# Kernel optimization log

Hardware: AMD Instinct MI355X
Metric: run time of the kernel (lower is better)

The kernel has to match this reference:

```python
import jax, jax.numpy as jnp
import numpy as np

N = 50000      # nodes
E = 800000     # edges (before self-loops)
F_IN = 64      # num_features
HID = 32       # hidden_channels
HEADS = 4
CLS = 3
NEG_SLOPE = 0.2  # PyG GATConv default


def setup_inputs() -> dict:
    key = jax.random.key(0)
    ks = jax.random.split(key, 12)
    s = 0.1
    return {
        "x": jax.random.normal(ks[0], (N, F_IN), jnp.float32),
        "W1": jax.random.normal(ks[1], (F_IN, HEADS * HID), jnp.float32) * s,
        "att_src1": jax.random.normal(ks[2], (HEADS, HID), jnp.float32) * s,
        "att_dst1": jax.random.normal(ks[3], (HEADS, HID), jnp.float32) * s,
        "b1": jnp.zeros((HEADS * HID,), jnp.float32),
        "W2": jax.random.normal(ks[4], (HEADS * HID, HID), jnp.float32) * s,
        "att_src2": jax.random.normal(ks[5], (1, HID), jnp.float32) * s,
        "att_dst2": jax.random.normal(ks[6], (1, HID), jnp.float32) * s,
        "b2": jnp.zeros((HID,), jnp.float32),
        "linW": jax.random.normal(ks[7], (HID, CLS), jnp.float32) * s,
        "linb": jnp.zeros((CLS,), jnp.float32),
        "edge_index": jax.random.randint(ks[8], (2, E), 0, N, dtype=jnp.int64),
    }


def _gat_conv(x, W, att_src, att_dst, bias, src, dst, heads):
    """PyG GATConv (eval mode, self-loops pre-added in src/dst)."""
    n = x.shape[0]
    h = (x @ W).reshape(n, heads, -1)                      # [N,H,C]
    a_src = jnp.sum(h * att_src, axis=-1)                  # [N,H]
    a_dst = jnp.sum(h * att_dst, axis=-1)                  # [N,H]
    e = jax.nn.leaky_relu(a_src[src] + a_dst[dst], NEG_SLOPE)  # [E,H]
    # segment softmax over destination node
    m = jax.ops.segment_max(e, dst, num_segments=n)
    p = jnp.exp(e - m[dst])
    denom = jax.ops.segment_sum(p, dst, num_segments=n)
    alpha = p / denom[dst]                                 # [E,H]
    msg = h[src] * alpha[:, :, None]                       # [E,H,C]
    out = jax.ops.segment_sum(msg, dst, num_segments=n)    # [N,H,C]
    return out.reshape(n, -1) + bias                       # concat heads


def reference(x, W1, att_src1, att_dst1, b1, W2, att_src2, att_dst2, b2, linW, linb, edge_index):
    n = x.shape[0]
    loop = jnp.arange(n, dtype=edge_index.dtype)
    src = jnp.concatenate([edge_index[0], loop])  # add self-loops (PyG default)
    dst = jnp.concatenate([edge_index[1], loop])
    h = _gat_conv(x, W1, att_src1, att_dst1, b1, src, dst, HEADS)
    h = jax.nn.elu(h)
    h = _gat_conv(h, W2, att_src2, att_dst2, b2, src, dst, 1)
    g = jnp.mean(h, axis=0, keepdims=True)        # batch is None path
    logits = g @ linW + linb                      # [1, CLS]
    return jax.nn.softmax(logits, axis=1)
```

## Files before the change

### kernel.cpp

```cpp
#include <hip/hip_runtime.h>
#include <hip/hip_fp16.h>
#include <math.h>

#define NEG_SLOPE 0.2f
#define CAP 64
#define SCB 2048

static __device__ __forceinline__ void atomAdd(float* a, float v) {
    unsafeAtomicAdd(a, v);
}

static __device__ __forceinline__ bool edges_are_i64(const int* __restrict__ ei) {
    return (ei[1] | ei[3] | ei[5] | ei[7]) == 0;
}
static __device__ __forceinline__ int ldsrc(const int* __restrict__ ei, int e, int E, bool i64) {
    return i64 ? ei[2 * e] : ei[e];
}
static __device__ __forceinline__ int lddst(const int* __restrict__ ei, int e, int E, bool i64) {
    return i64 ? ei[2 * (E + e)] : ei[E + e];
}

__global__ __launch_bounds__(256) void scatter_k(const int* __restrict__ ei,
                                                 int* __restrict__ deg,
                                                 int* __restrict__ col, int E, int N) {
    const int tid = threadIdx.x;
    const int grp = blockIdx.x & 3;
    const int bin = blockIdx.x >> 2;
    const int nb  = gridDim.x >> 2;
    const bool i64 = edges_are_i64(ei);
    const int ET = E + N;
    const int d0 = (int)((long long)grp * N / 4);
    const int d1 = (int)((long long)(grp + 1) * N / 4);
    for (int e = bin * 256 + tid; e < ET; e += nb * 256) {
        int s, d;
        if (e < E) { s = ldsrc(ei, e, E, i64); d = lddst(ei, e, E, i64); }
        else       { s = d = e - E; }
        if (d >= d0 && d < d1) {
            int pos = atomicAdd(&deg[d], 1);
            if (pos < CAP) col[d * CAP + pos] = s;
        }
    }
}

__global__ __launch_bounds__(256, 4) void gemm1_k(const float* __restrict__ x,
                                                  const float* __restrict__ W,
                                                  const float* __restrict__ aws,
                                                  const float* __restrict__ awd,
                                                  __half* __restrict__ h,
                                                  float* __restrict__ as_,
                                                  float* __restrict__ ad_, int N) {
    __shared__ float Ws[64 * 128];
    __shared__ float xs[32 * 64];
    const int tid = threadIdx.x;
    const int cg = tid & 31, rg = tid >> 5;
    const int r0 = blockIdx.x * 32;
#pragma unroll 1
    for (int i = tid; i < 8192; i += 256) Ws[i] = W[i];
    {
        const float* src = x + (size_t)r0 * 64;
        const int limit = (N - r0) * 64;
#pragma unroll 1
        for (int i = tid * 4; i < 2048; i += 1024) {
            float4 v = (i < limit) ? *(const float4*)(src + i) : make_float4(0, 0, 0, 0);
            *(float4*)(xs + i) = v;
        }
    }
    __syncthreads();

    float acc[4][4] = {};
#pragma unroll 2
    for (int k = 0; k < 64; k += 4) {
        float4 w0 = *(const float4*)(Ws + (k + 0) * 128 + cg * 4);
        float4 w1 = *(const float4*)(Ws + (k + 1) * 128 + cg * 4);
        float4 w2 = *(const float4*)(Ws + (k + 2) * 128 + cg * 4);
        float4 w3 = *(const float4*)(Ws + (k + 3) * 128 + cg * 4);
        float4 xv[4];
#pragma unroll
        for (int q = 0; q < 4; ++q) xv[q] = *(const float4*)(xs + (rg * 4 + q) * 64 + k);
#pragma unroll
        for (int q = 0; q < 4; ++q) {
            float4 xq = xv[q];
            acc[q][0] += xq.x * w0.x + xq.y * w1.x + xq.z * w2.x + xq.w * w3.x;
            acc[q][1] += xq.x * w0.y + xq.y * w1.y + xq.z * w2.y + xq.w * w3.y;
            acc[q][2] += xq.x * w0.z + xq.y * w1.z + xq.z * w2.z + xq.w * w3.z;
            acc[q][3] += xq.x * w0.w + xq.y * w1.w + xq.z * w2.w + xq.w * w3.w;
        }
    }

    const int jbase = cg * 4;
    const int head = cg >> 3;
    const float a0 = aws[jbase], a1 = aws[jbase + 1], a2 = aws[jbase + 2], a3 = aws[jbase + 3];
    const float d0 = awd[jbase], d1 = awd[jbase + 1], d2 = awd[jbase + 2], d3 = awd[jbase + 3];
    float ps[4], pd[4];
#pragma unroll
    for (int q = 0; q < 4; ++q) {
        ps[q] = acc[q][0] * a0 + acc[q][1] * a1 + acc[q][2] * a2 + acc[q][3] * a3;
        pd[q] = acc[q][0] * d0 + acc[q][1] * d1 + acc[q][2] * d2 + acc[q][3] * d3;
        int row = r0 + rg * 4 + q;
        if (row < N) {
            __half hv[4];
            hv[0] = __float2half(acc[q][0]); hv[1] = __float2half(acc[q][1]);
            hv[2] = __float2half(acc[q][2]); hv[3] = __float2half(acc[q][3]);
            *(uint2*)(h + (size_t)row * 128 + jbase) = *(uint2*)hv;
        }
    }
#pragma unroll
    for (int off = 4; off; off >>= 1) {
#pragma unroll
        for (int q = 0; q < 4; ++q) {
            ps[q] += __shfl_down(ps[q], off, 8);
            pd[q] += __shfl_down(pd[q], off, 8);
        }
    }
    if ((cg & 7) == 0) {
#pragma unroll
        for (int q = 0; q < 4; ++q) {
            int row = r0 + rg * 4 + q;
            if (row < N) { as_[row * 4 + head] = ps[q]; ad_[row * 4 + head] = pd[q]; }
        }
    }
}

__global__ __launch_bounds__(256, 4) void gemm2_k(const float* __restrict__ hact,
                                                  const float* __restrict__ W,
                                                  const float* __restrict__ aws,
                                                  const float* __restrict__ awd,
                                                  __half* __restrict__ h2,
                                                  float* __restrict__ as_,
                                                  float* __restrict__ ad_, int N) {
    __shared__ float Ws[128 * 32];
    __shared__ float xs[128 * 68];
    const int tid = threadIdx.x;
    const int cg = tid & 7, rg = tid >> 3;
    const int r0 = blockIdx.x * 128;
    for (int i = tid; i < 4096; i += 256) Ws[i] = W[i];

    float acc[4][4] = {};
#pragma unroll 1
    for (int p = 0; p < 2; ++p) {
        __syncthreads();
#pragma unroll 2
        for (int i = tid * 4; i < 8192; i += 1024) {
            int row = i >> 6, kk = i & 63;
            float4 v = (r0 + row < N)
                ? *(const float4*)(hact + (size_t)(r0 + row) * 128 + p * 64 + kk)
                : make_float4(0, 0, 0, 0);
            *(float4*)(xs + row * 68 + kk) = v;
        }
        __syncthreads();
#pragma unroll 2
        for (int k = 0; k < 64; k += 4) {
            float4 w0 = *(const float4*)(Ws + (p * 64 + k + 0) * 32 + cg * 4);
            float4 w1 = *(const float4*)(Ws + (p * 64 + k + 1) * 32 + cg * 4);
            float4 w2 = *(const float4*)(Ws + (p * 64 + k + 2) * 32 + cg * 4);
            float4 w3 = *(const float4*)(Ws + (p * 64 + k + 3) * 32 + cg * 4);
            float4 xv[4];
#pragma unroll
            for (int q = 0; q < 4; ++q) xv[q] = *(const float4*)(xs + (rg * 4 + q) * 68 + k);
#pragma unroll
            for (int q = 0; q < 4; ++q) {
                float4 xq = xv[q];
                acc[q][0] += xq.x * w0.x + xq.y * w1.x + xq.z * w2.x + xq.w * w3.x;
                acc[q][1] += xq.x * w0.y + xq.y * w1.y + xq.z * w2.y + xq.w * w3.y;
                acc[q][2] += xq.x * w0.z + xq.y * w1.z + xq.z * w2.z + xq.w * w3.z;
                acc[q][3] += xq.x * w0.w + xq.y * w1.w + xq.z * w2.w + xq.w * w3.w;
            }
        }
    }

    const int jbase = cg * 4;
    const float a0 = aws[jbase], a1 = aws[jbase + 1], a2 = aws[jbase + 2], a3 = aws[jbase + 3];
    const float d0 = awd[jbase], d1 = awd[jbase + 1], d2 = awd[jbase + 2], d3 = awd[jbase + 3];
    float ps[4], pd[4];
#pragma unroll
    for (int q = 0; q < 4; ++q) {
        ps[q] = acc[q][0] * a0 + acc[q][1] * a1 + acc[q][2] * a2 + acc[q][3] * a3;
        pd[q] = acc[q][0] * d0 + acc[q][1] * d1 + acc[q][2] * d2 + acc[q][3] * d3;
        int row = r0 + rg * 4 + q;
        if (row < N) {
            __half hv[4];
            hv[0] = __float2half(acc[q][0]); hv[1] = __float2half(acc[q][1]);
            hv[2] = __float2half(acc[q][2]); hv[3] = __float2half(acc[q][3]);
            *(uint2*)(h2 + (size_t)row * 32 + jbase) = *(uint2*)hv;
        }
    }
#pragma unroll
    for (int off = 4; off; off >>= 1) {
#pragma unroll
        for (int q = 0; q < 4; ++q) {
            ps[q] += __shfl_down(ps[q], off, 8);
            pd[q] += __shfl_down(pd[q], off, 8);
        }
    }
    if (cg == 0) {
#pragma unroll
        for (int q = 0; q < 4; ++q) {
            int row = r0 + rg * 4 + q;
            if (row < N) { as_[row] = ps[q]; ad_[row] = pd[q]; }
        }
    }
}

template <int ST>
static __device__ __forceinline__ void p1_wide(int s, float p, const __half* __restrict__ h,
                                               int half, int cl4, int hdA,
                                               float& a0, float& a1, float& a2, float& a3) {
    int su[ST]; float pu[ST]; uint2 g[ST];
#pragma unroll
    for (int u = 0; u < ST; ++u) su[u] = __shfl(s, 2 * u + half);
#pragma unroll
    for (int u = 0; u < ST; ++u) g[u] = *(const uint2*)(h + (size_t)su[u] * 128 + cl4 * 4);
#pragma unroll
    for (int u = 0; u < ST; ++u) pu[u] = __shfl(p, hdA * 16 + 2 * u + half);
#pragma unroll
    for (int u = 0; u < ST; ++u) {
        float2 f0 = __half22float2(*(const __half2*)&g[u].x);
        float2 f1 = __half22float2(*(const __half2*)&g[u].y);
        a0 += pu[u] * f0.x; a1 += pu[u] * f0.y;
        a2 += pu[u] * f1.x; a3 += pu[u] * f1.y;
    }
}

__global__ __launch_bounds__(256) void pull_agg1_k(const int* __restrict__ deg,
                                                   const int* __restrict__ col,
                                                   const float* __restrict__ asrc,
                                                   const float* __restrict__ adst,
                                                   const __half* __restrict__ h,
                                                   const float* __restrict__ b1,
                                                   float* __restrict__ hact, int N) {
    int wave = (blockIdx.x * 256 + threadIdx.x) >> 6;
    int lane = threadIdx.x & 63;
    if (wave >= N) return;
    const int d = wave;
    const int hd = lane >> 4;
    const int el = lane & 15;
    const int half = lane >> 5;
    const int cl4 = lane & 31;
    const int hdA = cl4 >> 3;
    const float ad = adst[d * 4 + hd];
    const int* cl = col + d * CAP;
    int cnt = deg[d]; if (cnt > CAP) cnt = CAP;
    float a0 = 0, a1 = 0, a2 = 0, a3 = 0, den = 0;

    for (int i = 0; i < cnt; i += 16) {
        const int r = cnt - i;
        int s = 0; float p = 0.0f;
        if (el < r) {
            s = cl[i + el];
            float v = asrc[s * 4 + hd] + ad;
            v = v > 0.0f ? v : NEG_SLOPE * v;
            p = __expf(v);
        }
        den += p;
        if (r > 8)      p1_wide<8>(s, p, h, half, cl4, hdA, a0, a1, a2, a3);
        else if (r > 4) p1_wide<4>(s, p, h, half, cl4, hdA, a0, a1, a2, a3);
        else            p1_wide<2>(s, p, h, half, cl4, hdA, a0, a1, a2, a3);
    }
    den += __shfl_xor(den, 1, 16);
    den += __shfl_xor(den, 2, 16);
    den += __shfl_xor(den, 4, 16);
    den += __shfl_xor(den, 8, 16);
    float denA = __shfl(den, hdA * 16);
    a0 += __shfl_xor(a0, 32);
    a1 += __shfl_xor(a1, 32);
    a2 += __shfl_xor(a2, 32);
    a3 += __shfl_xor(a3, 32);
    if (half == 0) {
        float inv = 1.0f / denA;
        float o0 = a0 * inv + b1[cl4 * 4 + 0];
        float o1 = a1 * inv + b1[cl4 * 4 + 1];
        float o2 = a2 * inv + b1[cl4 * 4 + 2];
        float o3 = a3 * inv + b1[cl4 * 4 + 3];
        o0 = o0 > 0.0f ? o0 : expm1f(o0);
        o1 = o1 > 0.0f ? o1 : expm1f(o1);
        o2 = o2 > 0.0f ? o2 : expm1f(o2);
        o3 = o3 > 0.0f ? o3 : expm1f(o3);
        *(float4*)(hact + (size_t)d * 128 + cl4 * 4) = make_float4(o0, o1, o2, o3);
    }
}

template <int NB>
static __device__ __forceinline__ void p2_batch(int s, float p, const __half* __restrict__ h,
                                                int lane, float& acc) {
    int su[NB];
#pragma unroll
    for (int u = 0; u < NB; ++u) su[u] = __shfl(s, u, 16);
    __half g[NB];
#pragma unroll
    for (int u = 0; u < NB; ++u) g[u] = h[(size_t)su[u] * 32 + lane];
    float pu[NB];
#pragma unroll
    for (int u = 0; u < NB; ++u) pu[u] = __shfl(p, u, 16);
#pragma unroll
    for (int u = 0; u < NB; ++u) acc += pu[u] * __half2float(g[u]);
}

__global__ __launch_bounds__(256) void pull_agg2_k(const int* __restrict__ deg,
                                                   const int* __restrict__ col,
                                                   const float* __restrict__ asrc,
                                                   const float* __restrict__ adst,
                                                   const __half* __restrict__ h,
                                                   float* __restrict__ gsum, int N) {
    const int tid = threadIdx.x;
    const int lane = tid & 31;
    const int el = lane & 15;
    const int gloc = tid >> 5;
    float csum = 0.0f;
    for (int d = blockIdx.x * 8 + gloc; d < N; d += gridDim.x * 8) {
        const float ad = adst[d];
        const int* cl = col + d * CAP;
        int cnt = deg[d]; if (cnt > CAP) cnt = CAP;
        float acc = 0.0f, den = 0.0f;
        for (int i = 0; i < cnt; i += 16) {
            const int r = cnt - i;
            int s = 0; float p = 0.0f;
            if (el < r) {
                s = cl[i + el];
                float v = asrc[s] + ad;
                v = v > 0.0f ? v : NEG_SLOPE * v;
                p = __expf(v);
            }
            den += p;
            p2_batch<16>(s, p, h, lane, acc);
        }
        den += __shfl_xor(den, 1, 16);
        den += __shfl_xor(den, 2, 16);
        den += __shfl_xor(den, 4, 16);
        den += __shfl_xor(den, 8, 16);
        csum += acc / den;
    }
    __shared__ float lds[256];
    lds[tid] = csum;
    __syncthreads();
    if (tid < 32) {
        float s2 = 0.0f;
#pragma unroll
        for (int g = 0; g < 8; ++g) s2 += lds[g * 32 + tid];
        atomAdd(&gsum[tid], s2);
    }
}

__global__ void final_k(const float* __restrict__ gsum, const float* __restrict__ b2w,
                        const float* __restrict__ linW, const float* __restrict__ linb,
                        float* __restrict__ out, int N) {
    if (threadIdx.x != 0 || blockIdx.x != 0) return;
    float g[32];
#pragma unroll
    for (int c = 0; c < 32; ++c) g[c] = gsum[c] / (float)N + b2w[c];
    float lo[3];
#pragma unroll
    for (int j = 0; j < 3; ++j) {
        float acc = linb[j];
#pragma unroll
        for (int c = 0; c < 32; ++c) acc += g[c] * linW[c * 3 + j];
        lo[j] = acc;
    }
    float mx = fmaxf(lo[0], fmaxf(lo[1], lo[2]));
    float ex[3], se = 0.0f;
#pragma unroll
    for (int j = 0; j < 3; ++j) { ex[j] = __expf(lo[j] - mx); se += ex[j]; }
#pragma unroll
    for (int j = 0; j < 3; ++j) out[j] = ex[j] / se;
}

extern "C" void kernel_launch(void* const* d_in, const int* in_sizes, int n_in,
                              void* d_out, int out_size, void* d_ws, size_t ws_size,
                              hipStream_t stream) {
    const float* x    = (const float*)d_in[0];
    const float* W1   = (const float*)d_in[1];
    const float* as1w = (const float*)d_in[2];
    const float* ad1w = (const float*)d_in[3];
    const float* b1   = (const float*)d_in[4];
    const float* W2   = (const float*)d_in[5];
    const float* as2w = (const float*)d_in[6];
    const float* ad2w = (const float*)d_in[7];
    const float* b2w  = (const float*)d_in[8];
    const float* linW = (const float*)d_in[9];
    const float* linb = (const float*)d_in[10];
    const int*   ei   = (const int*)d_in[11];

    const int N = in_sizes[0] / 64;
    const int E = in_sizes[11] / 2;

    float* ws = (float*)d_ws;
    __half* h1h  = (__half*)ws;
    float*  hact = ws + (size_t)N * 64;
    float* asrc1 = hact + (size_t)N * 128;
    float* adst1 = asrc1 + (size_t)N * 4;
    float* asrc2 = adst1 + (size_t)N * 4;
    float* adst2 = asrc2 + (size_t)N;
    float* gsum  = adst2 + (size_t)N;
    int* deg     = (int*)(gsum + 32);
    int* col     = deg + N;
    __half* h2h  = (__half*)ws;

    auto cdiv = [](int a, int b) { return (a + b - 1) / b; };

    hipMemsetAsync(gsum, 0, (size_t)(32 + N) * sizeof(int), stream);

    scatter_k<<<SCB, 256, 0, stream>>>(ei, deg, col, E, N);

    gemm1_k<<<cdiv(N, 32), 256, 0, stream>>>(x, W1, as1w, ad1w, h1h, asrc1, adst1, N);
    pull_agg1_k<<<cdiv(N, 4), 256, 0, stream>>>(deg, col, asrc1, adst1, h1h, b1, hact, N);

    gemm2_k<<<cdiv(N, 128), 256, 0, stream>>>(hact, W2, as2w, ad2w, h2h, asrc2, adst2, N);
    pull_agg2_k<<<2048, 256, 0, stream>>>(deg, col, asrc2, adst2, h2h, gsum, N);

    final_k<<<1, 64, 0, stream>>>(gsum, b2w, linW, linb, (float*)d_out, N);
}
```

Measured before the change: 242.7 us.

## Replace layer-2 gather aggregation with per-source weight scatter and weighted column sum

Because only the mean over nodes of the second GAT layer output is needed, the kernel now accumulates each source node's total normalized attention weight via atomics, then computes a weighted sum of h2 rows. This avoids gathering 32-wide h2 rows per edge. The cost is one extra kernel, extra atomics on a weight buffer, and a larger memset. The fixed 4x16 unroll assumes CAP is 64.

```diff
diff --git a/kernel.cpp b/kernel.cpp
--- a/kernel.cpp
+++ b/kernel.cpp
@@ -279,64 +279,61 @@
     }
 }
 
-template <int NB>
-static __device__ __forceinline__ void p2_batch(int s, float p, const __half* __restrict__ h,
-                                                int lane, float& acc) {
-    int su[NB];
-#pragma unroll
-    for (int u = 0; u < NB; ++u) su[u] = __shfl(s, u, 16);
-    __half g[NB];
-#pragma unroll
-    for (int u = 0; u < NB; ++u) g[u] = h[(size_t)su[u] * 32 + lane];
-    float pu[NB];
-#pragma unroll
-    for (int u = 0; u < NB; ++u) pu[u] = __shfl(p, u, 16);
-#pragma unroll
-    for (int u = 0; u < NB; ++u) acc += pu[u] * __half2float(g[u]);
-}
-
-__global__ __launch_bounds__(256) void pull_agg2_k(const int* __restrict__ deg,
-                                                   const int* __restrict__ col,
-                                                   const float* __restrict__ asrc,
-                                                   const float* __restrict__ adst,
-                                                   const __half* __restrict__ h,
-                                                   float* __restrict__ gsum, int N) {
+__global__ __launch_bounds__(256) void wpass_k(const int* __restrict__ deg,
+                                               const int* __restrict__ col,
+                                               const float* __restrict__ asrc,
+                                               const float* __restrict__ adst,
+                                               float* __restrict__ w, int N) {
     const int tid = threadIdx.x;
-    const int lane = tid & 31;
-    const int el = lane & 15;
-    const int gloc = tid >> 5;
-    float csum = 0.0f;
-    for (int d = blockIdx.x * 8 + gloc; d < N; d += gridDim.x * 8) {
+    const int el = tid & 15;
+    const int gloc = tid >> 4;
+    for (int d = blockIdx.x * 16 + gloc; d < N; d += gridDim.x * 16) {
         const float ad = adst[d];
         const int* cl = col + d * CAP;
         int cnt = deg[d]; if (cnt > CAP) cnt = CAP;
-        float acc = 0.0f, den = 0.0f;
-        for (int i = 0; i < cnt; i += 16) {
-            const int r = cnt - i;
+        float den = 0.0f;
+        int   sarr[4];
+        float parr[4];
+#pragma unroll
+        for (int b = 0; b < 4; ++b) {
+            const int i = b * 16;
             int s = 0; float p = 0.0f;
-            if (el < r) {
+            if (i + el < cnt) {
                 s = cl[i + el];
                 float v = asrc[s] + ad;
                 v = v > 0.0f ? v : NEG_SLOPE * v;
                 p = __expf(v);
             }
-            den += p;
-            p2_batch<16>(s, p, h, lane, acc);
+            sarr[b] = s; parr[b] = p; den += p;
         }
         den += __shfl_xor(den, 1, 16);
         den += __shfl_xor(den, 2, 16);
         den += __shfl_xor(den, 4, 16);
         den += __shfl_xor(den, 8, 16);
-        csum += acc / den;
-    }
+        const float inv = 1.0f / den;
+#pragma unroll
+        for (int b = 0; b < 4; ++b) {
+            if (parr[b] > 0.0f) atomAdd(&w[sarr[b]], parr[b] * inv);
+        }
+    }
+}
+
+__global__ __launch_bounds__(256) void colsum_k(const float* __restrict__ w,
+                                                const __half* __restrict__ h2,
+                                                float* __restrict__ gsum, int N) {
     __shared__ float lds[256];
-    lds[tid] = csum;
+    const int tid = threadIdx.x;
+    const int c = tid & 31, rg = tid >> 5;
+    float acc = 0.0f;
+    for (int r = blockIdx.x * 8 + rg; r < N; r += gridDim.x * 8)
+        acc += w[r] * __half2float(h2[(size_t)r * 32 + c]);
+    lds[tid] = acc;
     __syncthreads();
     if (tid < 32) {
-        float s2 = 0.0f;
-#pragma unroll
-        for (int g = 0; g < 8; ++g) s2 += lds[g * 32 + tid];
-        atomAdd(&gsum[tid], s2);
+        float s = 0.0f;
+#pragma unroll
+        for (int g = 0; g < 8; ++g) s += lds[g * 32 + tid];
+        atomAdd(&gsum[tid], s);
     }
 }
 
@@ -390,13 +387,14 @@
     float* asrc2 = adst1 + (size_t)N * 4;
     float* adst2 = asrc2 + (size_t)N;
     float* gsum  = adst2 + (size_t)N;
-    int* deg     = (int*)(gsum + 32);
+    float* wgt   = gsum + 32;
+    int* deg     = (int*)(wgt + N);
     int* col     = deg + N;
     __half* h2h  = (__half*)ws;
 
     auto cdiv = [](int a, int b) { return (a + b - 1) / b; };
 
-    hipMemsetAsync(gsum, 0, (size_t)(32 + N) * sizeof(int), stream);
+    hipMemsetAsync(gsum, 0, (size_t)(32 + 2 * N) * sizeof(int), stream);
 
     scatter_k<<<SCB, 256, 0, stream>>>(ei, deg, col, E, N);
 
@@ -404,7 +402,8 @@
     pull_agg1_k<<<cdiv(N, 4), 256, 0, stream>>>(deg, col, asrc1, adst1, h1h, b1, hact, N);
 
     gemm2_k<<<cdiv(N, 128), 256, 0, stream>>>(hact, W2, as2w, ad2w, h2h, asrc2, adst2, N);
-    pull_agg2_k<<<2048, 256, 0, stream>>>(deg, col, asrc2, adst2, h2h, gsum, N);
+    wpass_k<<<cdiv(N, 16), 256, 0, stream>>>(deg, col, asrc2, adst2, wgt, N);
+    colsum_k<<<256, 256, 0, stream>>>(wgt, h2h, gsum, N);
 
     final_k<<<1, 64, 0, stream>>>(gsum, b2w, linW, linb, (float*)d_out, N);
 }
```

Result: slower. 266.8 us (+9.9%).

## Store layer-1 features head-major and aggregate each head in separate blocks

Applied to the files above, without the earlier changes.

The layer-1 GEMM now writes its fp16 features head-major: one N×32 slab per head instead of interleaved 128-wide rows. The first aggregation is replaced by a grid-stride kernel in which each block handles a single head, with 16-lane groups processing one destination node each. The aim is a smaller gather working set per block (64 bytes per source row), which should improve L2 hit rates for the random source gathers. In exchange, the column list and degree are read four times, once per head, and the gathers become narrower 4-byte loads.

```diff
diff --git a/kernel.cpp b/kernel.cpp
--- a/kernel.cpp
+++ b/kernel.cpp
@@ -89,6 +89,8 @@
 
     const int jbase = cg * 4;
     const int head = cg >> 3;
+    const int chl  = (cg & 7) * 4;
+    const size_t slab = (size_t)N * 32;
     const float a0 = aws[jbase], a1 = aws[jbase + 1], a2 = aws[jbase + 2], a3 = aws[jbase + 3];
     const float d0 = awd[jbase], d1 = awd[jbase + 1], d2 = awd[jbase + 2], d3 = awd[jbase + 3];
     float ps[4], pd[4];
@@ -101,7 +103,7 @@
             __half hv[4];
             hv[0] = __float2half(acc[q][0]); hv[1] = __float2half(acc[q][1]);
             hv[2] = __float2half(acc[q][2]); hv[3] = __float2half(acc[q][3]);
-            *(uint2*)(h + (size_t)row * 128 + jbase) = *(uint2*)hv;
+            *(uint2*)(h + head * slab + (size_t)row * 32 + chl) = *(uint2*)hv;
         }
     }
 #pragma unroll
@@ -118,6 +120,72 @@
             int row = r0 + rg * 4 + q;
             if (row < N) { as_[row * 4 + head] = ps[q]; ad_[row * 4 + head] = pd[q]; }
         }
+    }
+}
+
+template <int NB>
+static __device__ __forceinline__ void ph_batch(int s, float p, const __half* __restrict__ hh,
+                                                int el, float& acc0, float& acc1) {
+    int su[NB]; unsigned g[NB]; float pu[NB];
+#pragma unroll
+    for (int u = 0; u < NB; ++u) su[u] = __shfl(s, u, 16);
+#pragma unroll
+    for (int u = 0; u < NB; ++u) g[u] = *(const unsigned*)(hh + (size_t)su[u] * 32 + el * 2);
+#pragma unroll
+    for (int u = 0; u < NB; ++u) pu[u] = __shfl(p, u, 16);
+#pragma unroll
+    for (int u = 0; u < NB; ++u) {
+        float2 f = __half22float2(*(const __half2*)&g[u]);
+        acc0 += pu[u] * f.x; acc1 += pu[u] * f.y;
+    }
+}
+
+__global__ __launch_bounds__(256) void pull_h_k(const int* __restrict__ deg,
+                                                const int* __restrict__ col,
+                                                const float* __restrict__ asrc,
+                                                const float* __restrict__ adst,
+                                                const __half* __restrict__ h,
+                                                const float* __restrict__ b1,
+                                                float* __restrict__ hact, int N) {
+    const int tid = threadIdx.x;
+    const int head = (blockIdx.x & 7) >> 1;
+    const int sub  = blockIdx.x & 1;
+    const int unit = tid >> 4;
+    const int el = tid & 15;
+    const size_t slab = (size_t)N * 32;
+    const __half* hh = h + head * slab;
+    const int nbh = (gridDim.x >> 3) * 2;
+    const float b0 = b1[head * 32 + el * 2];
+    const float b1v = b1[head * 32 + el * 2 + 1];
+    for (int d = ((blockIdx.x >> 3) * 2 + sub) * 16 + unit; d < N; d += nbh * 16) {
+        const float ad = adst[d * 4 + head];
+        const int* cl = col + d * CAP;
+        int cnt = deg[d]; if (cnt > CAP) cnt = CAP;
+        float acc0 = 0.0f, acc1 = 0.0f, den = 0.0f;
+        for (int i = 0; i < cnt; i += 16) {
+            const int r = cnt - i;
+            int s = 0; float p = 0.0f;
+            if (el < r) {
+                s = cl[i + el];
+                float v = asrc[s * 4 + head] + ad;
+                v = v > 0.0f ? v : NEG_SLOPE * v;
+                p = __expf(v);
+            }
+            den += p;
+            if (r > 8)      ph_batch<16>(s, p, hh, el, acc0, acc1);
+            else if (r > 4) ph_batch<8>(s, p, hh, el, acc0, acc1);
+            else            ph_batch<4>(s, p, hh, el, acc0, acc1);
+        }
+        den += __shfl_xor(den, 1, 16);
+        den += __shfl_xor(den, 2, 16);
+        den += __shfl_xor(den, 4, 16);
+        den += __shfl_xor(den, 8, 16);
+        float inv = 1.0f / den;
+        float o0 = acc0 * inv + b0;
+        float o1 = acc1 * inv + b1v;
+        o0 = o0 > 0.0f ? o0 : expm1f(o0);
+        o1 = o1 > 0.0f ? o1 : expm1f(o1);
+        *(float2*)(hact + (size_t)d * 128 + head * 32 + el * 2) = make_float2(o0, o1);
     }
 }
 
@@ -198,84 +266,6 @@
             int row = r0 + rg * 4 + q;
             if (row < N) { as_[row] = ps[q]; ad_[row] = pd[q]; }
         }
-    }
-}
-
-template <int ST>
-static __device__ __forceinline__ void p1_wide(int s, float p, const __half* __restrict__ h,
-                                               int half, int cl4, int hdA,
-                                               float& a0, float& a1, float& a2, float& a3) {
-    int su[ST]; float pu[ST]; uint2 g[ST];
-#pragma unroll
-    for (int u = 0; u < ST; ++u) su[u] = __shfl(s, 2 * u + half);
-#pragma unroll
-    for (int u = 0; u < ST; ++u) g[u] = *(const uint2*)(h + (size_t)su[u] * 128 + cl4 * 4);
-#pragma unroll
-    for (int u = 0; u < ST; ++u) pu[u] = __shfl(p, hdA * 16 + 2 * u + half);
-#pragma unroll
-    for (int u = 0; u < ST; ++u) {
-        float2 f0 = __half22float2(*(const __half2*)&g[u].x);
-        float2 f1 = __half22float2(*(const __half2*)&g[u].y);
-        a0 += pu[u] * f0.x; a1 += pu[u] * f0.y;
-        a2 += pu[u] * f1.x; a3 += pu[u] * f1.y;
-    }
-}
-
-__global__ __launch_bounds__(256) void pull_agg1_k(const int* __restrict__ deg,
-                                                   const int* __restrict__ col,
-                                                   const float* __restrict__ asrc,
-                                                   const float* __restrict__ adst,
-                                                   const __half* __restrict__ h,
-                                                   const float* __restrict__ b1,
-                                                   float* __restrict__ hact, int N) {
-    int wave = (blockIdx.x * 256 + threadIdx.x) >> 6;
-    int lane = threadIdx.x & 63;
-    if (wave >= N) return;
-    const int d = wave;
-    const int hd = lane >> 4;
-    const int el = lane & 15;
-    const int half = lane >> 5;
-    const int cl4 = lane & 31;
-    const int hdA = cl4 >> 3;
-    const float ad = adst[d * 4 + hd];
-    const int* cl = col + d * CAP;
-    int cnt = deg[d]; if (cnt > CAP) cnt = CAP;
-    float a0 = 0, a1 = 0, a2 = 0, a3 = 0, den = 0;
-
-    for (int i = 0; i < cnt; i += 16) {
-        const int r = cnt - i;
-        int s = 0; float p = 0.0f;
-        if (el < r) {
-            s = cl[i + el];
-            float v = asrc[s * 4 + hd] + ad;
-            v = v > 0.0f ? v : NEG_SLOPE * v;
-            p = __expf(v);
-        }
-        den += p;
-        if (r > 8)      p1_wide<8>(s, p, h, half, cl4, hdA, a0, a1, a2, a3);
-        else if (r > 4) p1_wide<4>(s, p, h, half, cl4, hdA, a0, a1, a2, a3);
-        else            p1_wide<2>(s, p, h, half, cl4, hdA, a0, a1, a2, a3);
-    }
-    den += __shfl_xor(den, 1, 16);
-    den += __shfl_xor(den, 2, 16);
-    den += __shfl_xor(den, 4, 16);
-    den += __shfl_xor(den, 8, 16);
-    float denA = __shfl(den, hdA * 16);
-    a0 += __shfl_xor(a0, 32);
-    a1 += __shfl_xor(a1, 32);
-    a2 += __shfl_xor(a2, 32);
-    a3 += __shfl_xor(a3, 32);
-    if (half == 0) {
-        float inv = 1.0f / denA;
-        float o0 = a0 * inv + b1[cl4 * 4 + 0];
-        float o1 = a1 * inv + b1[cl4 * 4 + 1];
-        float o2 = a2 * inv + b1[cl4 * 4 + 2];
-        float o3 = a3 * inv + b1[cl4 * 4 + 3];
-        o0 = o0 > 0.0f ? o0 : expm1f(o0);
-        o1 = o1 > 0.0f ? o1 : expm1f(o1);
-        o2 = o2 > 0.0f ? o2 : expm1f(o2);
-        o3 = o3 > 0.0f ? o3 : expm1f(o3);
-        *(float4*)(hact + (size_t)d * 128 + cl4 * 4) = make_float4(o0, o1, o2, o3);
     }
 }
 
@@ -401,7 +391,7 @@
     scatter_k<<<SCB, 256, 0, stream>>>(ei, deg, col, E, N);
 
     gemm1_k<<<cdiv(N, 32), 256, 0, stream>>>(x, W1, as1w, ad1w, h1h, asrc1, adst1, N);
-    pull_agg1_k<<<cdiv(N, 4), 256, 0, stream>>>(deg, col, asrc1, adst1, h1h, b1, hact, N);
+    pull_h_k<<<2048, 256, 0, stream>>>(deg, col, asrc1, adst1, h1h, b1, hact, N);
 
     gemm2_k<<<cdiv(N, 128), 256, 0, stream>>>(hact, W2, as2w, ad2w, h2h, asrc2, adst2, N);
     pull_agg2_k<<<2048, 256, 0, stream>>>(deg, col, asrc2, adst2, h2h, gsum, N);
```

Result: slower. 262.3 us (+8.1%).
